# Optimization experiments

Hardware: AMD Instinct MI355X
Metric: run time of the kernel (lower is better)

Reference implementation:

```python
import jax, jax.numpy as jnp
import numpy as np

NUM_GRAPHS = 128
NODES_PER_GRAPH = 512
N_NODES = NUM_GRAPHS * NODES_PER_GRAPH
N_EDGES = 524288
IN_DIM = 128
HID = 128
OUT_DIM = 10
N_LAYERS = 3
POOL_RATIO = 0.5  # TopKPooling default ratio


def setup_inputs() -> dict:
    key = jax.random.key(0)
    ks = jax.random.split(key, 16)
    x = jax.random.normal(ks[0], (N_NODES, IN_DIM), dtype=jnp.float32)
    edge_index = jax.random.randint(ks[1], (2, N_EDGES), 0, N_NODES, dtype=jnp.int64)
    batch = jnp.repeat(jnp.arange(NUM_GRAPHS, dtype=jnp.int64), NODES_PER_GRAPH)
    s = 0.05
    return {
        "x": x,
        "edge_index": edge_index,
        "batch": batch,
        "emb_W": jax.random.normal(ks[2], (IN_DIM, HID), dtype=jnp.float32) * s,
        "emb_b": jnp.zeros((HID,), dtype=jnp.float32),
        "gcn_W": jax.random.normal(ks[3], (N_LAYERS, HID, HID), dtype=jnp.float32) * s,
        "gcn_b": jnp.zeros((N_LAYERS, HID), dtype=jnp.float32),
        "pool_p": jax.random.normal(ks[4], (HID,), dtype=jnp.float32),
        "fc1_W": jax.random.normal(ks[5], (HID, 128), dtype=jnp.float32) * s,
        "fc1_b": jnp.zeros((128,), dtype=jnp.float32),
        "fc2_W": jax.random.normal(ks[6], (128, 64), dtype=jnp.float32) * s,
        "fc2_b": jnp.zeros((64,), dtype=jnp.float32),
        "fc3_W": jax.random.normal(ks[7], (64, OUT_DIM), dtype=jnp.float32) * s,
        "fc3_b": jnp.zeros((OUT_DIM,), dtype=jnp.float32),
    }


def reference(x, edge_index, batch, emb_W, emb_b, gcn_W, gcn_b, pool_p,
              fc1_W, fc1_b, fc2_W, fc2_b, fc3_W, fc3_b):
    n = x.shape[0]
    # embedding
    h = x @ emb_W + emb_b
    # GCNConv normalization (PyG semantics): add self loops, deg from target scatter
    loop = jnp.arange(n, dtype=edge_index.dtype)
    src = jnp.concatenate([edge_index[0], loop])
    dst = jnp.concatenate([edge_index[1], loop])
    deg = jax.ops.segment_sum(jnp.ones_like(src, dtype=h.dtype), dst, num_segments=n)
    dinv = jnp.where(deg > 0, jax.lax.rsqrt(jnp.maximum(deg, 1e-12)), 0.0)
    norm = dinv[src] * dinv[dst]  # [E+n]
    for l in range(gcn_W.shape[0]):
        hw = h @ gcn_W[l]                                   # [n, HID]
        msg = hw[src] * norm[:, None]                        # gather + scale
        h = jax.nn.relu(jax.ops.segment_sum(msg, dst, num_segments=n) + gcn_b[l])
    # TopKPooling (ratio=0.5, tanh nonlinearity), uniform graphs -> reshape + top_k
    npg = n // NUM_GRAPHS
    k = int(np.ceil(POOL_RATIO * npg))
    score = (h @ pool_p) / jnp.linalg.norm(pool_p)           # [n]
    score_g = score.reshape(NUM_GRAPHS, npg)
    topv, topi = jax.lax.top_k(score_g, k)                   # [G, k]
    h_g = h.reshape(NUM_GRAPHS, npg, -1)
    h_sel = jnp.take_along_axis(h_g, topi[:, :, None], axis=1) * jnp.tanh(topv)[:, :, None]
    pooled = h_sel.mean(axis=1)                              # global_mean_pool -> [G, HID]
    # MLP head (dropout is identity in eval)
    z = jax.nn.relu(pooled @ fc1_W + fc1_b)
    z = jax.nn.relu(z @ fc2_W + fc2_b)
    return z @ fc3_W + fc3_b
```

## Files before the change

kernel.cpp:

```cpp
#include <hip/hip_runtime.h>
#include <hip/hip_bf16.h>
#include <math.h>


static __device__ __forceinline__ float4 f4add(float4 a, float4 b) {
    return make_float4(a.x + b.x, a.y + b.y, a.z + b.z, a.w + b.w);
}
static __device__ __forceinline__ float4 f4fma(float s, float4 a, float4 acc) {
    return make_float4(fmaf(s, a.x, acc.x), fmaf(s, a.y, acc.y),
                       fmaf(s, a.z, acc.z), fmaf(s, a.w, acc.w));
}

__global__ __launch_bounds__(128) void fold_emb(
    const float* __restrict__ embW, const float* __restrict__ embb,
    const float* __restrict__ W0, float* __restrict__ W01,
    float* __restrict__ b01)
{
    const int r = blockIdx.x;
    const int c = threadIdx.x;
    __shared__ float rs[128];
    rs[c] = (r < 128) ? embW[r * 128 + c] : embb[c];
    __syncthreads();
    float s = 0.f;
#pragma unroll 8
    for (int k = 0; k < 128; k++) s = fmaf(rs[k], W0[k * 128 + c], s);
    if (r < 128) W01[r * 128 + c] = s;
    else         b01[c] = s;
}

#define ASTRIDE 257
#define WSTRIDE 140
__global__ __launch_bounds__(256) void gemm128(
    const float* __restrict__ A, const float* __restrict__ W,
    const float* __restrict__ bias, const float* __restrict__ rowscale,
    float* __restrict__ out, int n)
{
    __shared__ float As[32 * ASTRIDE];
    __shared__ float Ws[32 * WSTRIDE];
    const int tid  = threadIdx.x;
    const int rb   = blockIdx.x * 128;
    const int tc   = tid & 15;
    const int tr   = tid >> 4;
    const int colg = tc * 8;
    const int cswz = colg + ((colg >> 5) << 2);
    const int rowg = tr * 8;

    const int a_kq = tid & 7;
    const int a_m  = tid >> 3;
    const int w_c  = (tid & 31) * 4;
    const int w_cs = w_c + ((w_c >> 5) << 2);
    const int w_k  = tid >> 5;

    float acc[8][8];
#pragma unroll
    for (int i = 0; i < 8; i++)
#pragma unroll
        for (int j = 0; j < 8; j++) acc[i][j] = 0.f;

    float4 areg[4], wreg[4];
#pragma unroll
    for (int t = 0; t < 4; t++)
        areg[t] = *(const float4*)&A[(size_t)(rb + t * 32 + a_m) * 128 + a_kq * 4];
#pragma unroll
    for (int t = 0; t < 4; t++)
        wreg[t] = *(const float4*)&W[(size_t)(t * 8 + w_k) * 128 + w_c];

#pragma unroll 1
    for (int k0 = 0; k0 < 128; k0 += 32) {
#pragma unroll
        for (int t = 0; t < 4; t++) {
            const int m = t * 32 + a_m;
            const float4 av = areg[t];
            As[(a_kq * 4 + 0) * ASTRIDE + m] = av.x;
            As[(a_kq * 4 + 1) * ASTRIDE + m] = av.y;
            As[(a_kq * 4 + 2) * ASTRIDE + m] = av.z;
            As[(a_kq * 4 + 3) * ASTRIDE + m] = av.w;
        }
#pragma unroll
        for (int t = 0; t < 4; t++)
            *(float4*)&Ws[(t * 8 + w_k) * WSTRIDE + w_cs] = wreg[t];
        __syncthreads();
        if (k0 < 96) {
#pragma unroll
            for (int t = 0; t < 4; t++)
                areg[t] = *(const float4*)&A[(size_t)(rb + t * 32 + a_m) * 128 + k0 + 32 + a_kq * 4];
#pragma unroll
            for (int t = 0; t < 4; t++)
                wreg[t] = *(const float4*)&W[(size_t)(k0 + 32 + t * 8 + w_k) * 128 + w_c];
        }
#pragma unroll 8
        for (int kk = 0; kk < 32; kk++) {
            float4 a0 = *(const float4*)&As[kk * ASTRIDE + rowg];
            float4 a1 = *(const float4*)&As[kk * ASTRIDE + rowg + 4];
            float4 b0 = *(const float4*)&Ws[kk * WSTRIDE + cswz];
            float4 b1 = *(const float4*)&Ws[kk * WSTRIDE + cswz + 4];
            float av[8] = {a0.x, a0.y, a0.z, a0.w, a1.x, a1.y, a1.z, a1.w};
            float bv[8] = {b0.x, b0.y, b0.z, b0.w, b1.x, b1.y, b1.z, b1.w};
#pragma unroll
            for (int i = 0; i < 8; i++)
#pragma unroll
                for (int j = 0; j < 8; j++) acc[i][j] = fmaf(av[i], bv[j], acc[i][j]);
        }
        __syncthreads();
    }

    float4 bb0 = make_float4(0.f, 0.f, 0.f, 0.f), bb1 = bb0;
    if (bias) {
        bb0 = *(const float4*)&bias[colg];
        bb1 = *(const float4*)&bias[colg + 4];
    }
#pragma unroll
    for (int i = 0; i < 8; i++) {
        const int row  = rb + rowg + i;
        const float sc = rowscale ? rowscale[row] : 1.f;
        float4 o0, o1;
        o0.x = (acc[i][0] + bb0.x) * sc;  o0.y = (acc[i][1] + bb0.y) * sc;
        o0.z = (acc[i][2] + bb0.z) * sc;  o0.w = (acc[i][3] + bb0.w) * sc;
        o1.x = (acc[i][4] + bb1.x) * sc;  o1.y = (acc[i][5] + bb1.y) * sc;
        o1.z = (acc[i][6] + bb1.z) * sc;  o1.w = (acc[i][7] + bb1.w) * sc;
        *(float4*)&out[(size_t)row * 128 + colg]     = o0;
        *(float4*)&out[(size_t)row * 128 + colg + 4] = o1;
    }
}

__global__ void count_edges(const int* __restrict__ dst, int* __restrict__ cnt, int E)
{
    int e = blockIdx.x * blockDim.x + threadIdx.x;
    if (e < E) atomicAdd(&cnt[dst[e]], 1);
}

__global__ void scan1(const int* __restrict__ cnt, int* __restrict__ offs,
                      int* __restrict__ bsum, float* __restrict__ dinv)
{
    __shared__ int tmp[256];
    int t = threadIdx.x;
    int i = blockIdx.x * 256 + t;
    int v = cnt[i];
    dinv[i] = rsqrtf((float)(v + 1));
    tmp[t] = v;
    __syncthreads();
    for (int o = 1; o < 256; o <<= 1) {
        int add = (t >= o) ? tmp[t - o] : 0;
        __syncthreads();
        tmp[t] += add;
        __syncthreads();
    }
    offs[i] = tmp[t] - v;
    if (t == 255) bsum[blockIdx.x] = tmp[255];
}

__global__ void scan2(const int* __restrict__ bsum, int* __restrict__ boff)
{
    __shared__ int tmp[256];
    int t = threadIdx.x;
    int v = bsum[t];
    tmp[t] = v;
    __syncthreads();
    for (int o = 1; o < 256; o <<= 1) {
        int add = (t >= o) ? tmp[t - o] : 0;
        __syncthreads();
        tmp[t] += add;
        __syncthreads();
    }
    boff[t] = tmp[t] - v;
}

__global__ void scan3(int* __restrict__ offs, const int* __restrict__ boff,
                      int* __restrict__ cursor, int n, int E)
{
    int i = blockIdx.x * 256 + threadIdx.x;
    int v = offs[i] + boff[blockIdx.x];
    offs[i]   = v;
    cursor[i] = v;
    if (i == 0) offs[n] = E;
}

__global__ void scatter_edges(const int* __restrict__ src, const int* __restrict__ dst,
                              int* __restrict__ cursor, int* __restrict__ csr, int E)
{
    int e = blockIdx.x * blockDim.x + threadIdx.x;
    if (e < E) {
        int d   = dst[e];
        int pos = atomicAdd(&cursor[d], 1);
        csr[pos] = src[e];
    }
}

__global__ __launch_bounds__(256) void aggregate(
    const float* __restrict__ hs, const int* __restrict__ csr,
    const int* __restrict__ offs, const float* __restrict__ dinv,
    const float* __restrict__ bias, float* __restrict__ hout,
    const float* __restrict__ pool_p, float* __restrict__ scores, int n)
{
    const int grp  = threadIdx.x >> 5;
    const int lane = threadIdx.x & 31;
    const int node = blockIdx.x * 8 + grp;
    const float4* __restrict__ hv = (const float4*)hs;

    const int e0 = offs[node], e1 = offs[node + 1];

    int   ix[16];
    float mk[16];
#pragma unroll
    for (int j = 0; j < 16; j++) {
        const int  e  = e0 + j;
        const bool v  = e < e1;
        const int  ce = v ? e : (e1 > 0 ? e1 - 1 : 0);
        ix[j] = csr[ce];
        mk[j] = v ? 1.f : 0.f;
    }

    float4 self = hv[(size_t)node * 32 + lane];
    float4 r[16];
#pragma unroll
    for (int j = 0; j < 16; j++)
        r[j] = hv[(size_t)ix[j] * 32 + lane];
    asm volatile("" ::: "memory");

    float4 a0 = self;
    float4 a1 = make_float4(0.f, 0.f, 0.f, 0.f);
    float4 a2 = a1, a3 = a1;
#pragma unroll
    for (int j = 0; j < 16; j += 4) {
        a0 = f4fma(mk[j + 0], r[j + 0], a0);
        a1 = f4fma(mk[j + 1], r[j + 1], a1);
        a2 = f4fma(mk[j + 2], r[j + 2], a2);
        a3 = f4fma(mk[j + 3], r[j + 3], a3);
    }
    for (int e = e0 + 16; e < e1; e++) {
        a1 = f4add(a1, hv[(size_t)csr[e] * 32 + lane]);
    }

    float4 s = f4add(f4add(a0, a1), f4add(a2, a3));
    const float dv = dinv[node];
    const float4 bb = ((const float4*)bias)[lane];
    float4 o;
    o.x = fmaxf(fmaf(s.x, dv, bb.x), 0.f);
    o.y = fmaxf(fmaf(s.y, dv, bb.y), 0.f);
    o.z = fmaxf(fmaf(s.z, dv, bb.z), 0.f);
    o.w = fmaxf(fmaf(s.w, dv, bb.w), 0.f);
    ((float4*)hout)[(size_t)node * 32 + lane] = o;

    if (scores) {
        float4 pv = ((const float4*)pool_p)[lane];
        float d  = o.x * pv.x + o.y * pv.y + o.z * pv.z + o.w * pv.w;
        float nn = pv.x * pv.x + pv.y * pv.y + pv.z * pv.z + pv.w * pv.w;
#pragma unroll
        for (int off = 16; off > 0; off >>= 1) {
            d  += __shfl_xor(d, off);
            nn += __shfl_xor(nn, off);
        }
        if (lane == 0) scores[node] = d * rsqrtf(nn);
    }
}

__global__ __launch_bounds__(512) void topk_pool(
    const float* __restrict__ scores, const float* __restrict__ h,
    float* __restrict__ pooled)
{
    __shared__ float s[512];
    __shared__ int   sel[256];
    __shared__ float w[256];
    __shared__ float4 red[512];
    const int g = blockIdx.x;
    const int i = threadIdx.x;
    s[i] = scores[g * 512 + i];
    __syncthreads();
    float si = s[i];
    int rank = 0;
    for (int j = 0; j < 512; j++) {
        float sj = s[j];
        rank += (sj > si) || (sj == si && j < i);
    }
    if (rank < 256) {
        sel[rank] = i;
        w[rank]   = tanhf(si) * (1.f / 256.f);
    }
    __syncthreads();
    const int c   = (i & 31) * 4;
    const int grp = i >> 5;
    float4 acc = make_float4(0.f, 0.f, 0.f, 0.f);
    for (int t = grp; t < 256; t += 16) {
        float wt  = w[t];
        int   idx = sel[t];
        float4 r = *(const float4*)&h[((size_t)g * 512 + idx) * 128 + c];
        acc = f4fma(wt, r, acc);
    }
    red[i] = acc;
    __syncthreads();
    if (i < 256) red[i] = f4add(red[i], red[i + 256]);
    __syncthreads();
    if (i < 128) red[i] = f4add(red[i], red[i + 128]);
    __syncthreads();
    if (i < 64) red[i] = f4add(red[i], red[i + 64]);
    __syncthreads();
    if (i < 32) {
        float4 v = f4add(red[i], red[i + 32]);
        *(float4*)&pooled[g * 128 + i * 4] = v;
    }
}

__global__ __launch_bounds__(128) void mlp_head(
    const float* __restrict__ pooled,
    const float* __restrict__ fc1W, const float* __restrict__ fc1b,
    const float* __restrict__ fc2W, const float* __restrict__ fc2b,
    const float* __restrict__ fc3W, const float* __restrict__ fc3b,
    float* __restrict__ out)
{
    __shared__ float pld[128];
    __shared__ float z1[128];
    __shared__ float z2[64];
    int g = blockIdx.x, j = threadIdx.x;
    pld[j] = pooled[g * 128 + j];
    __syncthreads();
    float a = fc1b[j];
    for (int k = 0; k < 128; k++) a += pld[k] * fc1W[k * 128 + j];
    z1[j] = fmaxf(a, 0.f);
    __syncthreads();
    if (j < 64) {
        float b = fc2b[j];
        for (int k = 0; k < 128; k++) b += z1[k] * fc2W[k * 64 + j];
        z2[j] = fmaxf(b, 0.f);
    }
    __syncthreads();
    if (j < 10) {
        float o = fc3b[j];
        for (int k = 0; k < 64; k++) o += z2[k] * fc3W[k * 10 + j];
        out[g * 10 + j] = o;
    }
}

extern "C" void kernel_launch(void* const* d_in, const int* in_sizes, int n_in,
                              void* d_out, int out_size, void* d_ws, size_t ws_size,
                              hipStream_t stream)
{
    const float* x     = (const float*)d_in[0];
    const int*   eidx  = (const int*)d_in[1];
    const float* embW  = (const float*)d_in[3];
    const float* embb  = (const float*)d_in[4];
    const float* gcnW  = (const float*)d_in[5];
    const float* gcnb  = (const float*)d_in[6];
    const float* poolp = (const float*)d_in[7];
    const float* fc1W  = (const float*)d_in[8];
    const float* fc1b  = (const float*)d_in[9];
    const float* fc2W  = (const float*)d_in[10];
    const float* fc2b  = (const float*)d_in[11];
    const float* fc3W  = (const float*)d_in[12];
    const float* fc3b  = (const float*)d_in[13];
    float* out = (float*)d_out;

    const int n = in_sizes[0] / 128;
    const int E = in_sizes[1] / 2;
    const int G = n / 512;

    const int* src = eidx;
    const int* dst = eidx + E;

    char* ws = (char*)d_ws;
    size_t off = 0;
    auto carve = [&](size_t bytes) {
        void* p = ws + off;
        off += (bytes + 255) & ~(size_t)255;
        return p;
    };
    float* h      = (float*)carve((size_t)n * 128 * 4);
    float* hs     = (float*)carve((size_t)n * 128 * 4);
    float* dinv   = (float*)carve((size_t)n * 4);
    int*   cnt    = (int*)carve((size_t)n * 4);
    int*   offs   = (int*)carve((size_t)(n + 1) * 4);
    int*   cursor = (int*)carve((size_t)n * 4);
    int*   bsum   = (int*)carve(256 * 4);
    int*   boff   = (int*)carve(256 * 4);
    int*   csr    = (int*)carve((size_t)E * 4);
    float* scores = (float*)carve((size_t)n * 4);
    float* pooled = (float*)carve((size_t)G * 128 * 4);
    float* W01    = (float*)carve(128 * 128 * 4);
    float* b01    = (float*)carve(128 * 4);
    (void)ws_size;

    hipMemsetAsync(cnt, 0, (size_t)n * 4, stream);
    count_edges<<<E / 256, 256, 0, stream>>>(dst, cnt, E);
    scan1<<<n / 256, 256, 0, stream>>>(cnt, offs, bsum, dinv);
    scan2<<<1, 256, 0, stream>>>(bsum, boff);
    scan3<<<n / 256, 256, 0, stream>>>(offs, boff, cursor, n, E);
    scatter_edges<<<E / 256, 256, 0, stream>>>(src, dst, cursor, csr, E);

    fold_emb<<<129, 128, 0, stream>>>(embW, embb, gcnW, W01, b01);

    gemm128<<<n / 128, 256, 0, stream>>>(x, W01, b01, dinv, hs, n);
    aggregate<<<n / 8, 256, 0, stream>>>(hs, csr, offs, dinv, gcnb, h,
                                         poolp, nullptr, n);

    for (int l = 1; l < 3; l++) {
        gemm128<<<n / 128, 256, 0, stream>>>(h, gcnW + (size_t)l * 128 * 128,
                                             nullptr, dinv, hs, n);
        aggregate<<<n / 8, 256, 0, stream>>>(
            hs, csr, offs, dinv, gcnb + (size_t)l * 128, h,
            poolp, (l == 2) ? scores : nullptr, n);
    }

    topk_pool<<<G, 512, 0, stream>>>(scores, h, pooled);
    mlp_head<<<G, 128, 0, stream>>>(pooled, fc1W, fc1b, fc2W, fc2b, fc3W, fc3b, out);
}
```

Before: 430.5 us.

## Halve GEMM row tile to 64 and store A row-major in shared memory

The dense 128-wide GEMM now uses 64-row tiles with 128-thread blocks, doubling the grid. A is stored row-major in LDS with stride 33 instead of transposed, and the inner loop reads float4 chunks along k per row. W is loaded per k-chunk inside the loop without register prefetch. The aim is more blocks for occupancy and cheaper LDS stores, at the cost of more scalar-strided LDS reads of A, more reloads of W per output row, and less latency hiding on W.

```diff
diff --git a/kernel.cpp b/kernel.cpp
--- a/kernel.cpp
+++ b/kernel.cpp
@@ -28,17 +28,17 @@
     else         b01[c] = s;
 }
 
-#define ASTRIDE 257
-#define WSTRIDE 140
-__global__ __launch_bounds__(256) void gemm128(
+#define AST 33
+#define WST 140
+__global__ __launch_bounds__(128) void gemm128(
     const float* __restrict__ A, const float* __restrict__ W,
     const float* __restrict__ bias, const float* __restrict__ rowscale,
     float* __restrict__ out, int n)
 {
-    __shared__ float As[32 * ASTRIDE];
-    __shared__ float Ws[32 * WSTRIDE];
+    __shared__ float As[64 * AST];
+    __shared__ float Ws[32 * WST];
     const int tid  = threadIdx.x;
-    const int rb   = blockIdx.x * 128;
+    const int rb   = blockIdx.x * 64;
     const int tc   = tid & 15;
     const int tr   = tid >> 4;
     const int colg = tc * 8;
@@ -57,49 +57,50 @@
 #pragma unroll
         for (int j = 0; j < 8; j++) acc[i][j] = 0.f;
 
-    float4 areg[4], wreg[4];
+    float4 areg[4];
 #pragma unroll
     for (int t = 0; t < 4; t++)
-        areg[t] = *(const float4*)&A[(size_t)(rb + t * 32 + a_m) * 128 + a_kq * 4];
-#pragma unroll
-    for (int t = 0; t < 4; t++)
-        wreg[t] = *(const float4*)&W[(size_t)(t * 8 + w_k) * 128 + w_c];
+        areg[t] = *(const float4*)&A[(size_t)(rb + a_m + 16 * t) * 128 + a_kq * 4];
 
 #pragma unroll 1
     for (int k0 = 0; k0 < 128; k0 += 32) {
-#pragma unroll
-        for (int t = 0; t < 4; t++) {
-            const int m = t * 32 + a_m;
-            const float4 av = areg[t];
-            As[(a_kq * 4 + 0) * ASTRIDE + m] = av.x;
-            As[(a_kq * 4 + 1) * ASTRIDE + m] = av.y;
-            As[(a_kq * 4 + 2) * ASTRIDE + m] = av.z;
-            As[(a_kq * 4 + 3) * ASTRIDE + m] = av.w;
+        float4 wv[8];
+#pragma unroll
+        for (int t = 0; t < 8; t++)
+            wv[t] = *(const float4*)&W[(size_t)(k0 + w_k + 4 * t) * 128 + w_c];
+#pragma unroll
+        for (int t = 0; t < 4; t++)
+            *(float4*)&As[(a_m + 16 * t) * AST + a_kq * 4] = areg[t];
+#pragma unroll
+        for (int t = 0; t < 8; t++)
+            *(float4*)&Ws[(w_k + 4 * t) * WST + w_cs] = wv[t];
+        __syncthreads();
+        if (k0 < 96) {
+#pragma unroll
+            for (int t = 0; t < 4; t++)
+                areg[t] = *(const float4*)&A[(size_t)(rb + a_m + 16 * t) * 128 + k0 + 32 + a_kq * 4];
         }
 #pragma unroll
-        for (int t = 0; t < 4; t++)
-            *(float4*)&Ws[(t * 8 + w_k) * WSTRIDE + w_cs] = wreg[t];
-        __syncthreads();
-        if (k0 < 96) {
-#pragma unroll
-            for (int t = 0; t < 4; t++)
-                areg[t] = *(const float4*)&A[(size_t)(rb + t * 32 + a_m) * 128 + k0 + 32 + a_kq * 4];
-#pragma unroll
-            for (int t = 0; t < 4; t++)
-                wreg[t] = *(const float4*)&W[(size_t)(k0 + 32 + t * 8 + w_k) * 128 + w_c];
-        }
-#pragma unroll 8
-        for (int kk = 0; kk < 32; kk++) {
-            float4 a0 = *(const float4*)&As[kk * ASTRIDE + rowg];
-            float4 a1 = *(const float4*)&As[kk * ASTRIDE + rowg + 4];
-            float4 b0 = *(const float4*)&Ws[kk * WSTRIDE + cswz];
-            float4 b1 = *(const float4*)&Ws[kk * WSTRIDE + cswz + 4];
-            float av[8] = {a0.x, a0.y, a0.z, a0.w, a1.x, a1.y, a1.z, a1.w};
-            float bv[8] = {b0.x, b0.y, b0.z, b0.w, b1.x, b1.y, b1.z, b1.w};
+        for (int kq = 0; kq < 8; kq++) {
+            float4 a[8];
 #pragma unroll
             for (int i = 0; i < 8; i++)
-#pragma unroll
-                for (int j = 0; j < 8; j++) acc[i][j] = fmaf(av[i], bv[j], acc[i][j]);
+                a[i] = *(const float4*)&As[(rowg + i) * AST + kq * 4];
+            const float* af = (const float*)a;
+#pragma unroll
+            for (int k2 = 0; k2 < 4; k2++) {
+                const int k = kq * 4 + k2;
+                float4 b0 = *(const float4*)&Ws[k * WST + cswz];
+                float4 b1 = *(const float4*)&Ws[k * WST + cswz + 4];
+                float bv[8] = {b0.x, b0.y, b0.z, b0.w, b1.x, b1.y, b1.z, b1.w};
+#pragma unroll
+                for (int i = 0; i < 8; i++) {
+                    const float av = af[i * 4 + k2];
+#pragma unroll
+                    for (int j = 0; j < 8; j++)
+                        acc[i][j] = fmaf(av, bv[j], acc[i][j]);
+                }
+            }
         }
         __syncthreads();
     }
@@ -387,13 +388,13 @@
 
     fold_emb<<<129, 128, 0, stream>>>(embW, embb, gcnW, W01, b01);
 
-    gemm128<<<n / 128, 256, 0, stream>>>(x, W01, b01, dinv, hs, n);
+    gemm128<<<n / 64, 128, 0, stream>>>(x, W01, b01, dinv, hs, n);
     aggregate<<<n / 8, 256, 0, stream>>>(hs, csr, offs, dinv, gcnb, h,
                                          poolp, nullptr, n);
 
     for (int l = 1; l < 3; l++) {
-        gemm128<<<n / 128, 256, 0, stream>>>(h, gcnW + (size_t)l * 128 * 128,
-                                             nullptr, dinv, hs, n);
+        gemm128<<<n / 64, 128, 0, stream>>>(h, gcnW + (size_t)l * 128 * 128,
+                                            nullptr, dinv, hs, n);
         aggregate<<<n / 8, 256, 0, stream>>>(
             hs, csr, offs, dinv, gcnb + (size_t)l * 128, h,
             poolp, (l == 2) ? scores : nullptr, n);
```

Result: slower. 446.3 us (+3.7%).
